# Kernel tuning notes

Measured on AMD Instinct MI355X. Metric: run time of the kernel, lower is better.

Reference implementation:

```python
import jax, jax.numpy as jnp
import numpy as np

B, T, H, L, V = 256, 20, 512, 2, 8964
LQ, LH, LI = 40, 80, 49
BETA = 3.0


def setup_inputs() -> dict:
    key = jax.random.key(0)
    ks = iter(jax.random.split(key, 40))
    s = 1.0 / np.sqrt(H)
    n = lambda shape, sc=s: jax.random.normal(next(ks), shape, jnp.float32) * sc
    inp = {
        'emb': n((B, T, H), 1.0),
        'question': n((B, LQ, 2 * H), 1.0),
        'history': n((B, LH, 2 * H), 1.0),
        'image': n((B, LI, 2 * H), 1.0),
        'h0': jnp.zeros((L, B, H), jnp.float32),
        'c0': jnp.zeros((L, B, H), jnp.float32),
        # LSTM params (both layers have input dim H since ninp == nhid)
        'Wih': n((L, 4 * H, H)), 'Whh': n((L, 4 * H, H)),
        'bih': jnp.zeros((L, 4 * H), jnp.float32), 'bhh': jnp.zeros((L, 4 * H), jnp.float32),
        # question attention: w_q (2H->H), ans_q (H->H), Wa_q (H->1)
        'Wq': n((H, 2 * H)), 'bq': jnp.zeros((H,), jnp.float32),
        'Wansq': n((H, H)), 'bansq': jnp.zeros((H,), jnp.float32),
        'waq': n((1, H)), 'baq': jnp.zeros((1,), jnp.float32),
        # history attention
        'Wh': n((H, 2 * H)), 'bh': jnp.zeros((H,), jnp.float32),
        'Wansh': n((H, H)), 'bansh': jnp.zeros((H,), jnp.float32),
        'wah': n((1, H)), 'bah': jnp.zeros((1,), jnp.float32),
        # image attention
        'Wi': n((H, 2 * H)), 'bi': jnp.zeros((H,), jnp.float32),
        'Wansi': n((H, H)), 'bansi': jnp.zeros((H,), jnp.float32),
        'wai': n((1, H)), 'bai': jnp.zeros((1,), jnp.float32),
        # concat fusion (3H -> H)
        'Wcat': n((H, 3 * H)), 'bcat': jnp.zeros((H,), jnp.float32),
        # decoder SimpleClassifier: 2H -> 4H -> V
        'Wd1': n((4 * H, 2 * H)), 'bd1': jnp.zeros((4 * H,), jnp.float32),
        'Wd2': n((V, 4 * H), 1.0 / np.sqrt(4 * H)), 'bd2': jnp.zeros((V,), jnp.float32),
    }
    return inp


def reference(emb, question, history, image, h0, c0,
              Wih, Whh, bih, bhh,
              Wq, bq, Wansq, bansq, waq, baq,
              Wh, bh, Wansh, bansh, wah, bah,
              Wi, bi, Wansi, bansi, wai, bai,
              Wcat, bcat, Wd1, bd1, Wd2, bd2):
    nlayers = Wih.shape[0]
    # context projections are timestep-invariant: hoist out of the loop
    q_emb = question @ Wq.T + bq   # [B, LQ, H]
    h_emb = history @ Wh.T + bh    # [B, LH, H]
    i_emb = image @ Wi.T + bi      # [B, LI, H]

    def attend(ctx, out, Wans, bans, wa, ba):
        # ctx: [B, Lx, H], out: [B, H]
        a = jnp.tanh(ctx + (out @ Wans.T + bans)[:, None, :])
        logits = jnp.einsum('blh,h->bl', a, wa[0]) + ba[0]
        w = jax.nn.softmax(logits, axis=1)
        return jnp.einsum('bl,blh->bh', w, ctx)

    def step(carry, x_t):
        h, c = carry  # each [L, B, H]
        inp = x_t
        hs, cs = [], []
        for l in range(nlayers):
            gates = inp @ Wih[l].T + h[l] @ Whh[l].T + bih[l] + bhh[l]
            gi, gf, gg, go = jnp.split(gates, 4, axis=-1)  # torch gate order i,f,g,o
            cn = jax.nn.sigmoid(gf) * c[l] + jax.nn.sigmoid(gi) * jnp.tanh(gg)
            hn = jax.nn.sigmoid(go) * jnp.tanh(cn)
            hs.append(hn); cs.append(cn)
            inp = hn
        out = inp  # top-layer output [B, H]
        fq = attend(q_emb, out, Wansq, bansq, waq, baq)
        fh = attend(h_emb, out, Wansh, bansh, wah, bah)
        fi = attend(i_emb, out, Wansi, bansi, wai, bai)
        cat = jnp.tanh(jnp.concatenate([fq, fh, fi], axis=1) @ Wcat.T + bcat)
        fusion = jnp.concatenate([out, cat], axis=1)  # [B, 2H]
        dec = jax.nn.relu(fusion @ Wd1.T + bd1) @ Wd2.T + bd2
        lp = jax.nn.log_softmax(BETA * dec, axis=1)
        return (jnp.stack(hs), jnp.stack(cs)), lp

    (hT, cT), lps = jax.lax.scan(step, (h0, c0), jnp.swapaxes(emb, 0, 1))
    return jnp.swapaxes(lps, 0, 1), hT, cT
```

## Files before the change

kernel.cpp:

```cpp
#include <hip/hip_runtime.h>
#include <cmath>

#define B_ 256
#define T_ 20
#define H_ 512
#define V_ 8964
#define LQ_ 40
#define LH_ 80
#define LI_ 49
#define BT_ (B_ * T_)
#define BH_ (B_ * H_)
#define NPAD_ 9088
#define BETA_ 3.0f

#define MEGA_LSTM_ 128
#define MEGA_CTXQ_ 320
#define MEGA_CTXH_ 640
#define MEGA_CTXI_ 392
#define MEGA_CTX_ (MEGA_CTXQ_ + MEGA_CTXH_ + MEGA_CTXI_)
#define MEGA_GRID_ (MEGA_LSTM_ + MEGA_CTX_)

#define PREP_WCVT_ 2560
#define PREP_WD2_  9088
#define PREP_EMB_  1280
#define PREP_PERM_ 2048
#define PREP_H0_   128
#define PREP_BIAS_ 2
#define PREP_GRID_ (PREP_WCVT_ + PREP_WD2_ + PREP_EMB_ + PREP_PERM_ + PREP_H0_ + PREP_BIAS_)

typedef __attribute__((ext_vector_type(8))) short bf16x8;
typedef __attribute__((ext_vector_type(4))) float f32x4;
typedef __attribute__((ext_vector_type(8))) unsigned short u16x8;

static __device__ __forceinline__ unsigned short f2bf(float f) {
    union { float f; unsigned u; } v; v.f = f;
    unsigned r = v.u + 0x7FFF + ((v.u >> 16) & 1);
    return (unsigned short)(r >> 16);
}
static __device__ __forceinline__ float bf2f(unsigned short u) {
    union { unsigned u; float f; } v; v.u = ((unsigned)u) << 16;
    return v.f;
}
static __device__ __forceinline__ float fast_tanh(float x) {
    const float e = __expf(2.f * x);
    return 1.f - 2.f * __builtin_amdgcn_rcpf(e + 1.f);
}
static __device__ __forceinline__ float fast_sigmoid(float x) {
    return __builtin_amdgcn_rcpf(1.f + __expf(-x));
}
static __device__ __forceinline__ void st16_sc(unsigned short* p, unsigned short v) {
    unsigned int vv = v;
    asm volatile("global_store_short %0, %1, off sc0 sc1" :: "v"(p), "v"(vv) : "memory");
}
static __device__ __forceinline__ int ld32_sc(const int* p) {
    int v;
    asm volatile("global_load_dword %0, %1, off sc0 sc1\n\t"
                 "s_waitcnt vmcnt(0)"
                 : "=v"(v) : "v"(p) : "memory");
    return v;
}
#define GLD16(g, l) __builtin_amdgcn_global_load_lds(                                   \
    (const __attribute__((address_space(1))) unsigned int*)(unsigned long long)(const void*)(g), \
    (__attribute__((address_space(3))) unsigned int*)(unsigned int)(unsigned long long)(void*)(l), \
    16, 0, 0)

static __device__ __forceinline__ u16x8 cvt8(const float* p)
{
    float4 a = *reinterpret_cast<const float4*>(p);
    float4 b = *reinterpret_cast<const float4*>(p + 4);
    u16x8 v;
    v[0] = f2bf(a.x); v[1] = f2bf(a.y); v[2] = f2bf(a.z); v[3] = f2bf(a.w);
    v[4] = f2bf(b.x); v[5] = f2bf(b.y); v[6] = f2bf(b.z); v[7] = f2bf(b.w);
    return v;
}

struct PrepArgs {
    const float* wsrc[8]; unsigned short* wdst[8];
    const float* Wd2; unsigned short* Wd2p;
    const float* emb; unsigned short* emb_bf;
    const float* psrc[4]; unsigned short* pdst[4];
    const float* h0; unsigned short* hbuf;
    const float* bih; const float* bhh; float* bp0; float* bp1;
};

__global__ __launch_bounds__(256) void prep_kernel(PrepArgs a)
{
    static constexpr long long WSZ[8] = {524288, 524288, 524288, 262144,
                                         262144, 262144, 786432, 2097152};
    int g = blockIdx.x;
    const int tid = threadIdx.x;

    if (g < PREP_WCVT_) {
        long long off = (long long)g * 2048;
        int seg = 0;
#pragma unroll
        for (int i = 0; i < 8; ++i)
            if (seg == i && off >= WSZ[i]) { off -= WSZ[i]; ++seg; }
        const long long e = off + (long long)tid * 8;
        *reinterpret_cast<u16x8*>(a.wdst[seg] + e) = cvt8(a.wsrc[seg] + e);
        return;
    }
    g -= PREP_WCVT_;
    if (g < PREP_WD2_) {
        const long long e = (long long)g * 2048 + tid * 8;
        const long long row = e >> 11;
        u16x8 v;
        if (row < V_) v = cvt8(a.Wd2 + e);
        else v = (u16x8)0;
        *reinterpret_cast<u16x8*>(a.Wd2p + e) = v;
        return;
    }
    g -= PREP_WD2_;
    if (g < PREP_EMB_) {
        const long long e = (long long)g * 2048 + tid * 8;
        *reinterpret_cast<u16x8*>(a.emb_bf + e) = cvt8(a.emb + e);
        return;
    }
    g -= PREP_EMB_;
    if (g < PREP_PERM_) {
        const int which = g >> 9;
        const long long e0 = ((long long)(g & 511) * 256 + tid) * 8;
        const int drow = (int)(e0 >> 9);
        const int col = (int)(e0 & 511);
        const int gg = (drow >> 4) & 3;
        const int hsrc = ((drow >> 6) << 4) | (drow & 15);
        const int srow = (gg << 9) | hsrc;
        *reinterpret_cast<u16x8*>(a.pdst[which] + e0) =
            cvt8(a.psrc[which] + (long long)srow * 512 + col);
        return;
    }
    g -= PREP_PERM_;
    if (g < PREP_H0_) {
        const int half = g >> 6;
        const long long e = (long long)(g & 63) * 2048 + tid * 8;
        unsigned short* dst = a.hbuf + (half ? 4LL * BH_ : 0LL);
        *reinterpret_cast<u16x8*>(dst + e) = cvt8(a.h0 + (long long)half * BH_ + e);
        return;
    }
    g -= PREP_H0_;
    {
        const float* b1 = g ? a.bih + 2048 : a.bih;
        const float* b2 = g ? a.bhh + 2048 : a.bhh;
        float* dst = g ? a.bp1 : a.bp0;
#pragma unroll
        for (int i = 0; i < 8; ++i) {
            const int n = i * 256 + tid;
            const int gg = (n >> 4) & 3;
            const int h = ((n >> 6) << 4) | (n & 15);
            const int orig = (gg << 9) | h;
            dst[n] = b1[orig] + b2[orig];
        }
    }
}

static __device__ __forceinline__ int4 ldA8f(const float* A, long long idx)
{
    union { int4 i4; u16x8 v; } r;
    r.v = cvt8(A + idx);
    return r.i4;
}

template <int ACT, int OUTBF, int AF32>
__global__ __launch_bounds__(256, 2) void mfma_gemm(
    const void* __restrict__ A, const unsigned short* __restrict__ W,
    const float* __restrict__ bias1, const float* __restrict__ bias2,
    void* __restrict__ C, long long ldc, int Nreal, int K)
{
    __shared__ __align__(16) unsigned short As[2][128][32];
    __shared__ __align__(16) unsigned short Bs[2][128][32];
    const int tid = threadIdx.x;
    const int lane = tid & 63;
    const int wave = tid >> 6;
    const int wm = wave >> 1, wn = wave & 1;

    const int nwg = gridDim.x * gridDim.y;
    const int orig = blockIdx.y * gridDim.x + blockIdx.x;
    const int xcd = orig & 7, base = orig >> 3;
    const int q8 = nwg >> 3, r8 = nwg & 7;
    const int wg = (xcd < r8 ? xcd * (q8 + 1) : r8 * (q8 + 1) + (xcd - r8) * q8) + base;

    int MI = 8192 / (K << AF32);
    if (MI < 1) MI = 1;
    if (MI > (int)gridDim.y) MI = gridDim.y;
    const int slabSz = gridDim.x * MI;
    const int fullSlabs = gridDim.y / MI;
    const int fullRegion = fullSlabs * slabSz;
    int m0, n0;
    if (wg < fullRegion) {
        const int mb = wg / slabSz, rem = wg % slabSz;
        m0 = (mb * MI + rem % MI) * 128;
        n0 = (rem / MI) * 128;
    } else {
        const int rem = wg - fullRegion;
        const int TM = gridDim.y - fullSlabs * MI;
        m0 = (fullSlabs * MI + rem % TM) * 128;
        n0 = (rem / TM) * 128;
    }

    const int r = tid >> 2;
    const int ck = (tid & 3) * 8;

    const unsigned short* Wp = W + (long long)n0 * K;

    f32x4 acc[4][4] = {};
    int cur = 0;

    if constexpr (!AF32) {
        const unsigned short* Ab = (const unsigned short*)A;
        auto issue = [&](int k0, int buf) {
            const unsigned short* ga0 = Ab + (long long)(m0 + r) * K + k0 + ck;
            const unsigned short* ga1 = Ab + (long long)(m0 + r + 64) * K + k0 + ck;
            const unsigned short* gb0 = Wp + (long long)r * K + k0 + ck;
            const unsigned short* gb1 = Wp + (long long)(r + 64) * K + k0 + ck;
            char* lA = (char*)&As[buf][0][0] + wave * 1024;
            char* lB = (char*)&Bs[buf][0][0] + wave * 1024;
            GLD16(ga0, lA);
            GLD16(ga1, lA + 4096);
            GLD16(gb0, lB);
            GLD16(gb1, lB + 4096);
        };
        issue(0, 0);
        for (int k0 = 0; k0 < K; k0 += 32, cur ^= 1) {
            __syncthreads();
            if (k0 + 32 < K) issue(k0 + 32, cur ^ 1);
            const int lr = lane & 15, lk = (lane >> 4) * 8;
            bf16x8 af[4], bfr[4];
#pragma unroll
            for (int i = 0; i < 4; ++i) {
                af[i]  = *reinterpret_cast<const bf16x8*>(&As[cur][wm * 64 + i * 16 + lr][lk]);
                bfr[i] = *reinterpret_cast<const bf16x8*>(&Bs[cur][wn * 64 + i * 16 + lr][lk]);
            }
#pragma unroll
            for (int i = 0; i < 4; ++i)
#pragma unroll
                for (int j = 0; j < 4; ++j)
                    acc[i][j] = __builtin_amdgcn_mfma_f32_16x16x32_bf16(
                        af[i], bfr[j], acc[i][j], 0, 0, 0);
        }
    } else {
        const float* Af = (const float*)A;
        int4 ra0, ra1, rb0, rb1;
        ra0 = ldA8f(Af, (long long)(m0 + r) * K + ck);
        ra1 = ldA8f(Af, (long long)(m0 + r + 64) * K + ck);
        rb0 = *reinterpret_cast<const int4*>(Wp + (long long)r * K + ck);
        rb1 = *reinterpret_cast<const int4*>(Wp + (long long)(r + 64) * K + ck);
        for (int k0 = 0; k0 < K; k0 += 32, cur ^= 1) {
            *reinterpret_cast<int4*>(&As[cur][r][ck]) = ra0;
            *reinterpret_cast<int4*>(&As[cur][r + 64][ck]) = ra1;
            *reinterpret_cast<int4*>(&Bs[cur][r][ck]) = rb0;
            *reinterpret_cast<int4*>(&Bs[cur][r + 64][ck]) = rb1;
            __syncthreads();
            if (k0 + 32 < K) {
                const int kn = k0 + 32 + ck;
                ra0 = ldA8f(Af, (long long)(m0 + r) * K + kn);
                ra1 = ldA8f(Af, (long long)(m0 + r + 64) * K + kn);
                rb0 = *reinterpret_cast<const int4*>(Wp + (long long)r * K + kn);
                rb1 = *reinterpret_cast<const int4*>(Wp + (long long)(r + 64) * K + kn);
            }
            const int lr = lane & 15, lk = (lane >> 4) * 8;
            bf16x8 af[4], bfr[4];
#pragma unroll
            for (int i = 0; i < 4; ++i) {
                af[i]  = *reinterpret_cast<const bf16x8*>(&As[cur][wm * 64 + i * 16 + lr][lk]);
                bfr[i] = *reinterpret_cast<const bf16x8*>(&Bs[cur][wn * 64 + i * 16 + lr][lk]);
            }
#pragma unroll
            for (int i = 0; i < 4; ++i)
#pragma unroll
                for (int j = 0; j < 4; ++j)
                    acc[i][j] = __builtin_amdgcn_mfma_f32_16x16x32_bf16(
                        af[i], bfr[j], acc[i][j], 0, 0, 0);
        }
    }

    const int lr = lane & 15, lrow4 = (lane >> 4) * 4;
#pragma unroll
    for (int j = 0; j < 4; ++j) {
        const int col = n0 + wn * 64 + j * 16 + lr;
        if (col >= Nreal) continue;
        float bsum = 0.f;
        if (bias1) bsum += bias1[col];
        if (bias2) bsum += bias2[col];
#pragma unroll
        for (int i = 0; i < 4; ++i) {
#pragma unroll
            for (int rr = 0; rr < 4; ++rr) {
                const int row = m0 + wm * 64 + i * 16 + lrow4 + rr;
                float v = acc[i][j][rr] + bsum;
                if (ACT == 1) v = fast_tanh(v);
                if (ACT == 2) v = fmaxf(v, 0.f);
                if (OUTBF)
                    ((unsigned short*)C)[(long long)row * ldc + col] = f2bf(v);
                else
                    ((float*)C)[(long long)row * ldc + col] = v;
            }
        }
    }
}

static void mgemm(hipStream_t s, int act, int outbf, int af32,
                  const void* A, const unsigned short* W,
                  const float* b1, const float* b2,
                  void* C, long long ldc, int M, int Nreal, int K)
{
    dim3 grid((Nreal + 127) / 128, M / 128), blk(256);
#define MG(a, o, f) mfma_gemm<a, o, f><<<grid, blk, 0, s>>>(A, W, b1, b2, C, ldc, Nreal, K)
    if (af32) {
        if (outbf) { if (act == 1) MG(1,1,1); else if (act == 2) MG(2,1,1); else MG(0,1,1); }
        else       { if (act == 1) MG(1,0,1); else if (act == 2) MG(2,0,1); else MG(0,0,1); }
    } else {
        if (outbf) { if (act == 1) MG(1,1,0); else if (act == 2) MG(2,1,0); else MG(0,1,0); }
        else       { if (act == 1) MG(1,0,0); else if (act == 2) MG(2,0,0); else MG(0,0,0); }
    }
#undef MG
}

#define LSTM_ISSUE(b_, dst_) do {                                              \
    const unsigned short* pa_ = (((b_) >> 2) ? q20 : q10) + ((b_) & 3) * 128;  \
    const unsigned short* pb_ = (((b_) >> 2) ? q21 : q11) + ((b_) & 3) * 128;  \
    asm volatile(                                                              \
        "global_load_dwordx4 %0, %[pa], off sc0 sc1\n\t"                       \
        "global_load_dwordx4 %1, %[pa], off offset:64 sc0 sc1\n\t"             \
        "global_load_dwordx4 %2, %[pa], off offset:128 sc0 sc1\n\t"            \
        "global_load_dwordx4 %3, %[pa], off offset:192 sc0 sc1\n\t"            \
        "global_load_dwordx4 %4, %[pb], off sc0 sc1\n\t"                       \
        "global_load_dwordx4 %5, %[pb], off offset:64 sc0 sc1\n\t"             \
        "global_load_dwordx4 %6, %[pb], off offset:128 sc0 sc1\n\t"            \
        "global_load_dwordx4 %7, %[pb], off offset:192 sc0 sc1"                \
        : "=&v"((dst_)[0]), "=&v"((dst_)[1]), "=&v"((dst_)[2]), "=&v"((dst_)[3]), \
          "=&v"((dst_)[4]), "=&v"((dst_)[5]), "=&v"((dst_)[6]), "=&v"((dst_)[7])  \
        : [pa] "v"(pa_), [pb] "v"(pb_)                                         \
        : "memory");                                                           \
} while (0)

__global__ __launch_bounds__(256, 1) void mega_kernel(
    const unsigned short* __restrict__ emb_bf,
    const unsigned short* __restrict__ Wih0p, const unsigned short* __restrict__ Whh0p,
    const unsigned short* __restrict__ Wih1p, const unsigned short* __restrict__ Whh1p,
    const float* __restrict__ bp0, const float* __restrict__ bp1,
    const float* __restrict__ c0,
    unsigned short* __restrict__ hbuf,
    float* __restrict__ st_h, float* __restrict__ st_c,
    unsigned short* __restrict__ h_top,
    int* flags,
    const float* __restrict__ question, const float* __restrict__ history,
    const float* __restrict__ image,
    const unsigned short* __restrict__ Wq_bf, const unsigned short* __restrict__ Wh_bf,
    const unsigned short* __restrict__ Wi_bf,
    const float* __restrict__ bq, const float* __restrict__ bhb,
    const float* __restrict__ bi,
    unsigned short* __restrict__ q_emb, unsigned short* __restrict__ h_emb,
    unsigned short* __restrict__ i_emb)
{
    __shared__ __align__(16) char smem[131072];
    const int gid = blockIdx.x;
    const int tid = threadIdx.x;

    if (gid >= MEGA_LSTM_) {
        int g = gid - MEGA_LSTM_;
        const float* A; const unsigned short* W; const float* bias;
        unsigned short* Cc;
        if (g < MEGA_CTXQ_)       { A = question; W = Wq_bf; bias = bq;  Cc = q_emb; }
        else if (g < MEGA_CTXQ_ + MEGA_CTXH_) {
            g -= MEGA_CTXQ_;        A = history;  W = Wh_bf; bias = bhb; Cc = h_emb; }
        else { g -= MEGA_CTXQ_ + MEGA_CTXH_; A = image; W = Wi_bf; bias = bi; Cc = i_emb; }
        const int m0 = (g >> 2) * 128, n0 = (g & 3) * 128;
        const int K = 1024;

        unsigned short (*As)[128][32] = (unsigned short (*)[128][32])smem;
        unsigned short (*Bs)[128][32] = (unsigned short (*)[128][32])(smem + 16384);
        const int lane = tid & 63;
        const int wave = tid >> 6;
        const int wm = wave >> 1, wn = wave & 1;
        const int r = tid >> 2;
        const int ck = (tid & 3) * 8;
        const unsigned short* Wp = W + (long long)n0 * K;

        f32x4 acc[4][4] = {};
        int4 ra0, ra1, rb0, rb1;
        ra0 = ldA8f(A, (long long)(m0 + r) * K + ck);
        ra1 = ldA8f(A, (long long)(m0 + r + 64) * K + ck);
        rb0 = *reinterpret_cast<const int4*>(Wp + (long long)r * K + ck);
        rb1 = *reinterpret_cast<const int4*>(Wp + (long long)(r + 64) * K + ck);
        int cur = 0;
        for (int k0 = 0; k0 < K; k0 += 32, cur ^= 1) {
            *reinterpret_cast<int4*>(&As[cur][r][ck]) = ra0;
            *reinterpret_cast<int4*>(&As[cur][r + 64][ck]) = ra1;
            *reinterpret_cast<int4*>(&Bs[cur][r][ck]) = rb0;
            *reinterpret_cast<int4*>(&Bs[cur][r + 64][ck]) = rb1;
            __syncthreads();
            if (k0 + 32 < K) {
                const int kn = k0 + 32 + ck;
                ra0 = ldA8f(A, (long long)(m0 + r) * K + kn);
                ra1 = ldA8f(A, (long long)(m0 + r + 64) * K + kn);
                rb0 = *reinterpret_cast<const int4*>(Wp + (long long)r * K + kn);
                rb1 = *reinterpret_cast<const int4*>(Wp + (long long)(r + 64) * K + kn);
            }
            const int lr = lane & 15, lk = (lane >> 4) * 8;
            bf16x8 af[4], bfr[4];
#pragma unroll
            for (int i = 0; i < 4; ++i) {
                af[i]  = *reinterpret_cast<const bf16x8*>(&As[cur][wm * 64 + i * 16 + lr][lk]);
                bfr[i] = *reinterpret_cast<const bf16x8*>(&Bs[cur][wn * 64 + i * 16 + lr][lk]);
            }
#pragma unroll
            for (int i = 0; i < 4; ++i)
#pragma unroll
                for (int j = 0; j < 4; ++j)
                    acc[i][j] = __builtin_amdgcn_mfma_f32_16x16x32_bf16(
                        af[i], bfr[j], acc[i][j], 0, 0, 0);
        }
        const int lr = lane & 15, lrow4 = (lane >> 4) * 4;
#pragma unroll
        for (int j = 0; j < 4; ++j) {
            const int col = n0 + wn * 64 + j * 16 + lr;
            const float bsum = bias[col];
#pragma unroll
            for (int i = 0; i < 4; ++i)
#pragma unroll
                for (int rr = 0; rr < 4; ++rr) {
                    const int row = m0 + wm * 64 + i * 16 + lrow4 + rr;
                    Cc[(long long)row * 512 + col] = f2bf(acc[i][j][rr] + bsum);
                }
        }
        return;
    }

    const int grp = gid >> 6;
    const int id  = gid & 63;
    const int mt = id >> 5, nt = id & 31;
    const int m0 = mt * 128, n0 = nt * 64;
    const int lane = tid & 63;
    const int w = tid >> 6;
    const int lr = lane & 15;
    const int hi = lane >> 4;
    const int hi4 = hi * 4;

    const unsigned short* W1g = (grp ? Wih1p : Wih0p) + (long long)n0 * H_;
    const unsigned short* W2g = (grp ? Whh1p : Whh0p) + (long long)n0 * H_;

#pragma unroll
    for (int it = 0; it < 16; ++it) {
        const int e = (tid + it * 256) * 8;
        const int row = e >> 9, col = e & 511;
        const int bir = (col * 2) ^ ((row & 7) << 4);
        char* dst = smem + row * 1024 + bir;
        *reinterpret_cast<int4*>(dst) =
            *reinterpret_cast<const int4*>(W1g + (long long)row * H_ + col);
        *reinterpret_cast<int4*>(dst + 65536) =
            *reinterpret_cast<const int4*>(W2g + (long long)row * H_ + col);
    }
    __syncthreads();

    const int h = nt * 16 + lr;
    const float* bp = grp ? bp1 : bp0;
    float bg[4];
#pragma unroll
    for (int g = 0; g < 4; ++g) bg[g] = bp[n0 + g * 16 + lr];

    const int ar0 = m0 + w * 32 + lr;
    const int ar1 = ar0 + 16;

    float cregA[4], cregB[4], hn0[4], hn1[4];
#pragma unroll
    for (int rr = 0; rr < 4; ++rr) {
        cregA[rr] = c0[(long long)grp * BH_ + (long long)(m0 + w * 32 + hi4 + rr) * H_ + h];
        cregB[rr] = c0[(long long)grp * BH_ + (long long)(m0 + w * 32 + 16 + hi4 + rr) * H_ + h];
    }

    int bbase[4];
#pragma unroll
    for (int j = 0; j < 4; ++j)
        bbase[j] = (j * 16 + lr) * 1024 + ((hi * 16) ^ ((lr & 3) << 4));
    const int xk6 = ((lr >> 2) & 1) << 6;

    int* myFlag = flags + (mt * 64 + grp * 32 + nt) * 16;
    const long long sEmb = (long long)T_ * H_;

    for (int s = 0; s <= T_; ++s) {
        const bool active = (grp == 0) ? (s < T_) : (s >= 1);
        const int t = grp ? (s - 1) : s;
        if (active) {
            const unsigned short *A1, *A2;
            long long sA1;
            unsigned short* hout;
            if (grp == 0) {
                A1 = emb_bf + (long long)t * H_; sA1 = sEmb;
                A2 = hbuf + (long long)(s % 3) * BH_;
                hout = hbuf + (long long)((s + 1) % 3) * BH_;
            } else {
                A1 = hbuf + (long long)(s % 3) * BH_; sA1 = H_;
                A2 = hbuf + (long long)(3 + (s & 1)) * BH_;
                hout = hbuf + (long long)(3 + ((s + 1) & 1)) * BH_;
            }
            const unsigned short* q10 = A1 + (long long)ar0 * sA1 + hi * 8;
            const unsigned short* q11 = A1 + (long long)ar1 * sA1 + hi * 8;
            const unsigned short* q20 = A2 + (long long)ar0 * H_ + hi * 8;
            const unsigned short* q21 = A2 + (long long)ar1 * H_ + hi * 8;

            int4 buf[3][8];
            LSTM_ISSUE(0, buf[0]);
            LSTM_ISSUE(1, buf[1]);
            LSTM_ISSUE(2, buf[2]);

            f32x4 accA[4] = {}, accB[4] = {};
#pragma unroll
            for (int b = 0; b < 8; ++b) {
                if (b < 6)      asm volatile("s_waitcnt vmcnt(16)" ::: "memory");
                else if (b == 6) asm volatile("s_waitcnt vmcnt(8)" ::: "memory");
                else             asm volatile("s_waitcnt vmcnt(0)" ::: "memory");
                __builtin_amdgcn_sched_barrier(0);
#pragma unroll
                for (int i = 0; i < 4; ++i) {
                    const int it = b * 4 + i;
                    const int kk = it & 15, p = it >> 4;
                    const bf16x8 a0 = *reinterpret_cast<const bf16x8*>(&buf[b % 3][i]);
                    const bf16x8 a1 = *reinterpret_cast<const bf16x8*>(&buf[b % 3][4 + i]);
                    const int kb = ((kk << 6) ^ xk6) + (p << 16);
#pragma unroll
                    for (int j = 0; j < 4; ++j) {
                        const bf16x8 bfv = *reinterpret_cast<const bf16x8*>(
                            smem + bbase[j] + kb);
                        accA[j] = __builtin_amdgcn_mfma_f32_16x16x32_bf16(a0, bfv, accA[j], 0, 0, 0);
                        accB[j] = __builtin_amdgcn_mfma_f32_16x16x32_bf16(a1, bfv, accB[j], 0, 0, 0);
                    }
                }
                if (b + 3 < 8) LSTM_ISSUE(b + 3, buf[b % 3]);
            }

#pragma unroll
            for (int rr = 0; rr < 4; ++rr) {
                {
                    const int b = m0 + w * 32 + hi4 + rr;
                    const float i_ = fast_sigmoid(accA[0][rr] + bg[0]);
                    const float f_ = fast_sigmoid(accA[1][rr] + bg[1]);
                    const float g_ = fast_tanh(accA[2][rr] + bg[2]);
                    const float o_ = fast_sigmoid(accA[3][rr] + bg[3]);
                    const float cn = f_ * cregA[rr] + i_ * g_;
                    const float hn = o_ * fast_tanh(cn);
                    cregA[rr] = cn; hn0[rr] = hn;
                    st16_sc(&hout[(long long)b * H_ + h], f2bf(hn));
                }
                {
                    const int b = m0 + w * 32 + 16 + hi4 + rr;
                    const float i_ = fast_sigmoid(accB[0][rr] + bg[0]);
                    const float f_ = fast_sigmoid(accB[1][rr] + bg[1]);
                    const float g_ = fast_tanh(accB[2][rr] + bg[2]);
                    const float o_ = fast_sigmoid(accB[3][rr] + bg[3]);
                    const float cn = f_ * cregB[rr] + i_ * g_;
                    const float hn = o_ * fast_tanh(cn);
                    cregB[rr] = cn; hn1[rr] = hn;
                    st16_sc(&hout[(long long)b * H_ + h], f2bf(hn));
                }
            }
            if (s == T_) {
#pragma unroll
                for (int rr = 0; rr < 4; ++rr) {
                    const int b0r = m0 + w * 32 + hi4 + rr;
                    const int b1r = b0r + 16;
                    h_top[((long long)b0r * T_ + t) * H_ + h] = f2bf(hn0[rr]);
                    h_top[((long long)b1r * T_ + t) * H_ + h] = f2bf(hn1[rr]);
                    st_h[(long long)grp * BH_ + (long long)b0r * H_ + h] = hn0[rr];
                    st_h[(long long)grp * BH_ + (long long)b1r * H_ + h] = hn1[rr];
                    st_c[(long long)grp * BH_ + (long long)b0r * H_ + h] = cregA[rr];
                    st_c[(long long)grp * BH_ + (long long)b1r * H_ + h] = cregB[rr];
                }
            }
        }
        if (s < T_) {
            __syncthreads();
            if (tid == 0) {
                int v = s + 1;
                asm volatile("global_store_dword %0, %1, off sc0 sc1"
                             :: "v"(myFlag), "v"(v) : "memory");
            }
            if (active) {
#pragma unroll
                for (int rr = 0; rr < 4; ++rr) {
                    const int b0r = m0 + w * 32 + hi4 + rr;
                    const int b1r = b0r + 16;
                    if (grp == 1) {
                        h_top[((long long)b0r * T_ + t) * H_ + h] = f2bf(hn0[rr]);
                        h_top[((long long)b1r * T_ + t) * H_ + h] = f2bf(hn1[rr]);
                    }
                    if (t == T_ - 1) {
                        st_h[(long long)grp * BH_ + (long long)b0r * H_ + h] = hn0[rr];
                        st_h[(long long)grp * BH_ + (long long)b1r * H_ + h] = hn1[rr];
                        st_c[(long long)grp * BH_ + (long long)b0r * H_ + h] = cregA[rr];
                        st_c[(long long)grp * BH_ + (long long)b1r * H_ + h] = cregB[rr];
                    }
                }
            }
            if (tid < 64) {
                const int thr = (grp == 0 && tid >= 32) ? s : s + 1;
                const int* fp = flags + (mt * 64 + tid) * 16;
                while (ld32_sc(fp) < thr) __builtin_amdgcn_s_sleep(2);
            }
            __syncthreads();
        }
    }
}

__global__ __launch_bounds__(256) void attend3_kernel(
    const unsigned short* __restrict__ q_emb, const unsigned short* __restrict__ h_emb,
    const unsigned short* __restrict__ i_emb,
    const float* __restrict__ proj3,
    const float* __restrict__ waq, const float* __restrict__ baq, const float* __restrict__ bansq,
    const float* __restrict__ wah, const float* __restrict__ bah, const float* __restrict__ bansh,
    const float* __restrict__ wai, const float* __restrict__ bai, const float* __restrict__ bansi,
    const unsigned short* __restrict__ h_top,
    unsigned short* __restrict__ fcat, unsigned short* __restrict__ fusion)
{
    __shared__ float p_lds[512];
    __shared__ float wa_lds[512];
    __shared__ float lg[96];
    const int bt0 = blockIdx.x;
    const int bt = (bt0 & 7) * (BT_ / 8) + (bt0 >> 3);
    const int c = blockIdx.y;
    const int b = bt / T_;
    const int tid = threadIdx.x;
    const int wid = tid >> 6, lane = tid & 63;

    if (c == 0 && tid < 64)
        *reinterpret_cast<u16x8*>(&fusion[(long long)bt * 1024 + tid * 8]) =
            *reinterpret_cast<const u16x8*>(&h_top[(long long)bt * 512 + tid * 8]);

    const unsigned short* ctx = c == 0 ? q_emb : c == 1 ? h_emb : i_emb;
    const int Lx = c == 0 ? LQ_ : c == 1 ? LH_ : LI_;
    const float* wa = c == 0 ? waq : c == 1 ? wah : wai;
    const float bav = (c == 0 ? baq : c == 1 ? bah : bai)[0];
    const float* bans = c == 0 ? bansq : c == 1 ? bansh : bansi;

    p_lds[tid]       = proj3[(long long)bt * 1536 + c * 512 + tid] + bans[tid];
    p_lds[tid + 256] = proj3[(long long)bt * 1536 + c * 512 + tid + 256] + bans[tid + 256];
    wa_lds[tid] = wa[tid];
    wa_lds[tid + 256] = wa[tid + 256];
    __syncthreads();

    for (int l = wid; l < Lx; l += 4) {
        const unsigned short* crow = ctx + ((long long)b * Lx + l) * H_;
        float acc = 0.f;
#pragma unroll
        for (int j = 0; j < 8; ++j) {
            const int hp = lane + 64 * j;
            acc += wa_lds[hp] * fast_tanh(bf2f(crow[hp]) + p_lds[hp]);
        }
        for (int o = 32; o > 0; o >>= 1) acc += __shfl_down(acc, o);
        if (lane == 0) lg[l] = acc + bav;
    }
    __syncthreads();
    if (tid == 0) {
        float m = -1e30f;
        for (int l = 0; l < Lx; ++l) m = fmaxf(m, lg[l]);
        float ssum = 0.f;
        for (int l = 0; l < Lx; ++l) { const float e = __expf(lg[l] - m); lg[l] = e; ssum += e; }
        const float inv = __builtin_amdgcn_rcpf(ssum);
        for (int l = 0; l < Lx; ++l) lg[l] *= inv;
    }
    __syncthreads();
    for (int hp = tid; hp < H_; hp += 256) {
        float acc = 0.f;
        for (int l = 0; l < Lx; ++l)
            acc += lg[l] * bf2f(ctx[((long long)b * Lx + l) * H_ + hp]);
        fcat[(long long)bt * 1536 + c * 512 + hp] = f2bf(acc);
    }
}

__global__ __launch_bounds__(256) void log_softmax_kernel(float* __restrict__ out)
{
    __shared__ float red[4];
    __shared__ float bc;
    const long long base = (long long)blockIdx.x * V_;
    const int tid = threadIdx.x, lane = tid & 63, wid = tid >> 6;

    float r[36];
    float m = -1e30f;
#pragma unroll
    for (int i = 0; i < 36; ++i) {
        const int v = tid + i * 256;
        r[i] = (v < V_) ? BETA_ * out[base + v] : -1e30f;
        m = fmaxf(m, r[i]);
    }
    for (int o = 32; o > 0; o >>= 1) m = fmaxf(m, __shfl_down(m, o));
    if (lane == 0) red[wid] = m;
    __syncthreads();
    if (tid == 0)
        bc = fmaxf(fmaxf(red[0], red[1]), fmaxf(red[2], red[3]));
    __syncthreads();
    m = bc;

    float s = 0.f;
#pragma unroll
    for (int i = 0; i < 36; ++i) s += __expf(r[i] - m);
    for (int o = 32; o > 0; o >>= 1) s += __shfl_down(s, o);
    if (lane == 0) red[wid] = s;
    __syncthreads();
    if (tid == 0) bc = m + logf(red[0] + red[1] + red[2] + red[3]);
    __syncthreads();
    const float ls = bc;
#pragma unroll
    for (int i = 0; i < 36; ++i) {
        const int v = tid + i * 256;
        if (v < V_) out[base + v] = r[i] - ls;
    }
}

extern "C" void kernel_launch(void* const* d_in, const int* in_sizes, int n_in,
                              void* d_out_, int out_size, void* d_ws, size_t ws_size,
                              hipStream_t stream)
{
    const float* emb      = (const float*)d_in[0];
    const float* question = (const float*)d_in[1];
    const float* history  = (const float*)d_in[2];
    const float* image    = (const float*)d_in[3];
    const float* h0       = (const float*)d_in[4];
    const float* c0       = (const float*)d_in[5];
    const float* Wih      = (const float*)d_in[6];
    const float* Whh      = (const float*)d_in[7];
    const float* bih      = (const float*)d_in[8];
    const float* bhh      = (const float*)d_in[9];
    const float* Wq    = (const float*)d_in[10]; const float* bq    = (const float*)d_in[11];
    const float* Wansq = (const float*)d_in[12]; const float* bansq = (const float*)d_in[13];
    const float* waq   = (const float*)d_in[14]; const float* baq   = (const float*)d_in[15];
    const float* Wh    = (const float*)d_in[16]; const float* bh    = (const float*)d_in[17];
    const float* Wansh = (const float*)d_in[18]; const float* bansh = (const float*)d_in[19];
    const float* wah   = (const float*)d_in[20]; const float* bah   = (const float*)d_in[21];
    const float* Wi    = (const float*)d_in[22]; const float* bi    = (const float*)d_in[23];
    const float* Wansi = (const float*)d_in[24]; const float* bansi = (const float*)d_in[25];
    const float* wai   = (const float*)d_in[26]; const float* bai   = (const float*)d_in[27];
    const float* Wcat  = (const float*)d_in[28]; const float* bcat  = (const float*)d_in[29];
    const float* Wd1   = (const float*)d_in[30]; const float* bd1   = (const float*)d_in[31];
    const float* Wd2   = (const float*)d_in[32]; const float* bd2   = (const float*)d_in[33];

    float* out = (float*)d_out_;

    int*   flags = (int*)d_ws;
    float* st_h = (float*)((char*)d_ws + 8192);
    float* st_c = st_h + 2LL * BH_;
    float* bp0  = st_c + 2LL * BH_;
    float* bp1  = bp0 + 2048;
    unsigned short* hbuf   = (unsigned short*)(bp1 + 2048);
    unsigned short* Wih0p  = hbuf + 5LL * BH_;
    unsigned short* Whh0p  = Wih0p + 2048LL * H_;
    unsigned short* Wih1p  = Whh0p + 2048LL * H_;
    unsigned short* Whh1p  = Wih1p + 2048LL * H_;
    unsigned short* emb_bf = Whh1p + 2048LL * H_;
    unsigned short* h_top_bf = emb_bf + (long long)BT_ * H_;
    unsigned short* q_emb_bf = h_top_bf + (long long)BT_ * H_;
    unsigned short* h_emb_bf = q_emb_bf + (long long)B_ * LQ_ * H_;
    unsigned short* i_emb_bf = h_emb_bf + (long long)B_ * LH_ * H_;
    unsigned short* dec1_bf  = i_emb_bf + (long long)B_ * LI_ * H_;
    unsigned short* Wd2p_bf  = dec1_bf + (long long)BT_ * 4 * H_;

    unsigned short* Wq_bf    = (unsigned short*)out;
    unsigned short* Wh_bf    = Wq_bf + 524288;
    unsigned short* Wi_bf    = Wh_bf + 524288;
    unsigned short* Wansq_bf = Wi_bf + 524288;
    unsigned short* Wansh_bf = Wansq_bf + 262144;
    unsigned short* Wansi_bf = Wansh_bf + 262144;
    unsigned short* Wcat_bf  = Wansi_bf + 262144;
    unsigned short* Wd1_bf   = Wcat_bf + 786432;
    float* proj3 = (float*)(Wd1_bf + 2097152);
    unsigned short* fcat_bf   = (unsigned short*)(proj3 + (long long)BT_ * 1536);
    unsigned short* fusion_bf = fcat_bf + (long long)BT_ * 1536;

    {
        PrepArgs a;
        a.wsrc[0] = Wq;    a.wdst[0] = Wq_bf;
        a.wsrc[1] = Wh;    a.wdst[1] = Wh_bf;
        a.wsrc[2] = Wi;    a.wdst[2] = Wi_bf;
        a.wsrc[3] = Wansq; a.wdst[3] = Wansq_bf;
        a.wsrc[4] = Wansh; a.wdst[4] = Wansh_bf;
        a.wsrc[5] = Wansi; a.wdst[5] = Wansi_bf;
        a.wsrc[6] = Wcat;  a.wdst[6] = Wcat_bf;
        a.wsrc[7] = Wd1;   a.wdst[7] = Wd1_bf;
        a.Wd2 = Wd2; a.Wd2p = Wd2p_bf;
        a.emb = emb; a.emb_bf = emb_bf;
        a.psrc[0] = Wih;               a.pdst[0] = Wih0p;
        a.psrc[1] = Whh;               a.pdst[1] = Whh0p;
        a.psrc[2] = Wih + 2048LL * H_; a.pdst[2] = Wih1p;
        a.psrc[3] = Whh + 2048LL * H_; a.pdst[3] = Whh1p;
        a.h0 = h0; a.hbuf = hbuf;
        a.bih = bih; a.bhh = bhh; a.bp0 = bp0; a.bp1 = bp1;
        prep_kernel<<<dim3(PREP_GRID_), dim3(256), 0, stream>>>(a);
    }
    hipMemsetAsync(flags, 0, 8192, stream);

    mega_kernel<<<dim3(MEGA_GRID_), dim3(256), 0, stream>>>(
        emb_bf, Wih0p, Whh0p, Wih1p, Whh1p, bp0, bp1, c0,
        hbuf, st_h, st_c, h_top_bf, flags,
        question, history, image, Wq_bf, Wh_bf, Wi_bf, bq, bh, bi,
        q_emb_bf, h_emb_bf, i_emb_bf);

    mgemm(stream, 0, 0, 0, h_top_bf, Wansq_bf, nullptr, nullptr, proj3, 1536, BT_, 1536, H_);
    attend3_kernel<<<dim3(BT_, 3), dim3(256), 0, stream>>>(
        q_emb_bf, h_emb_bf, i_emb_bf, proj3,
        waq, baq, bansq, wah, bah, bansh, wai, bai, bansi,
        h_top_bf, fcat_bf, fusion_bf);

    mgemm(stream, 1, 1, 0, fcat_bf, Wcat_bf, bcat, nullptr, fusion_bf + H_, 2 * H_, BT_, H_, 3 * H_);

    mgemm(stream, 2, 1, 0, fusion_bf, Wd1_bf, bd1, nullptr, dec1_bf, 4 * H_, BT_, 4 * H_, 2 * H_);
    mgemm(stream, 0, 0, 0, dec1_bf, Wd2p_bf, bd2, nullptr, out, V_, BT_, V_, 4 * H_);

    log_softmax_kernel<<<dim3(BT_), dim3(256), 0, stream>>>(out);

    hipMemcpyAsync(out + (long long)BT_ * V_, st_h,
                   4LL * BH_ * sizeof(float), hipMemcpyDeviceToDevice, stream);
}
```

Baseline: 912.9 us.

## Add 256x256-tile double-buffered GEMM with XCD-aware swizzle for vocab projection

```diff
diff --git a/kernel.cpp b/kernel.cpp
--- a/kernel.cpp
+++ b/kernel.cpp
@@ -10,7 +10,7 @@
 #define LI_ 49
 #define BT_ (B_ * T_)
 #define BH_ (B_ * H_)
-#define NPAD_ 9088
+#define NPAD_ 9216
 #define BETA_ 3.0f
 
 #define MEGA_LSTM_ 128
@@ -21,7 +21,7 @@
 #define MEGA_GRID_ (MEGA_LSTM_ + MEGA_CTX_)
 
 #define PREP_WCVT_ 2560
-#define PREP_WD2_  9088
+#define PREP_WD2_  9216
 #define PREP_EMB_  1280
 #define PREP_PERM_ 2048
 #define PREP_H0_   128
@@ -313,6 +313,122 @@
         else       { if (act == 1) MG(1,0,0); else if (act == 2) MG(2,0,0); else MG(0,0,0); }
     }
 #undef MG
+}
+
+__global__ __launch_bounds__(512, 1) void gemm256_kernel(
+    const unsigned short* __restrict__ A, const unsigned short* __restrict__ W,
+    const float* __restrict__ bias, float* __restrict__ C)
+{
+    __shared__ __align__(16) unsigned short As[2][256][64];
+    __shared__ __align__(16) unsigned short Bs[2][256][64];
+    const int tid = threadIdx.x;
+    const int lane = tid & 63;
+    const int wave = tid >> 6;
+    const int wm = wave >> 2, wn = wave & 3;
+    const int lr = lane & 15, hi = lane >> 4;
+    const int K = 2048;
+
+    const int nwg = gridDim.x * gridDim.y;
+    const int orig = blockIdx.y * gridDim.x + blockIdx.x;
+    const int xcd = orig & 7, base = orig >> 3;
+    const int q8 = nwg >> 3, r8 = nwg & 7;
+    const int wg = (xcd < r8 ? xcd * (q8 + 1) : r8 * (q8 + 1) + (xcd - r8) * q8) + base;
+    const int MI = 2;
+    const int slabSz = gridDim.x * MI;
+    int m0, n0;
+    {
+        const int mb = wg / slabSz, rem = wg % slabSz;
+        m0 = (mb * MI + rem % MI) * 256;
+        n0 = (rem / MI) * 256;
+    }
+
+    const int srow = lane >> 3;
+    const int scol = (lane & 7) * 8;
+    auto stage = [&](int kt, int b) {
+#pragma unroll
+        for (int q = 0; q < 4; ++q) {
+            const int c = wave * 4 + q;
+            const unsigned short* ga = A + (long long)(m0 + 8 * c + srow) * K + kt * 64 + scol;
+            GLD16(ga, (char*)&As[b][0][0] + c * 1024);
+        }
+#pragma unroll
+        for (int q = 0; q < 4; ++q) {
+            const int c = wave * 4 + q;
+            const unsigned short* gw = W + (long long)(n0 + 8 * c + srow) * K + kt * 64 + scol;
+            GLD16(gw, (char*)&Bs[b][0][0] + c * 1024);
+        }
+    };
+
+    f32x4 acc[8][4] = {};
+    const int nt = K / 64;
+    stage(0, 0);
+    stage(1, 1);
+
+    for (int t = 0; t < nt; ++t) {
+        const int b = t & 1;
+        if (t + 1 < nt) asm volatile("s_waitcnt vmcnt(8)" ::: "memory");
+        else            asm volatile("s_waitcnt vmcnt(0)" ::: "memory");
+        __builtin_amdgcn_s_barrier();
+
+#pragma unroll
+        for (int p = 0; p < 3; ++p) {
+            const int mh = p & 1, ks = p >> 1;
+            bf16x8 af[4], bfr[4];
+#pragma unroll
+            for (int i = 0; i < 4; ++i) {
+                af[i]  = *reinterpret_cast<const bf16x8*>(
+                    &As[b][wm * 128 + mh * 64 + i * 16 + lr][ks * 32 + hi * 8]);
+                bfr[i] = *reinterpret_cast<const bf16x8*>(
+                    &Bs[b][wn * 64 + i * 16 + lr][ks * 32 + hi * 8]);
+            }
+            __builtin_amdgcn_s_setprio(1);
+#pragma unroll
+            for (int i = 0; i < 4; ++i)
+#pragma unroll
+                for (int j = 0; j < 4; ++j)
+                    acc[mh * 4 + i][j] = __builtin_amdgcn_mfma_f32_16x16x32_bf16(
+                        af[i], bfr[j], acc[mh * 4 + i][j], 0, 0, 0);
+            __builtin_amdgcn_s_setprio(0);
+            __builtin_amdgcn_s_barrier();
+        }
+        {
+            bf16x8 af[4], bfr[4];
+#pragma unroll
+            for (int i = 0; i < 4; ++i) {
+                af[i]  = *reinterpret_cast<const bf16x8*>(
+                    &As[b][wm * 128 + 64 + i * 16 + lr][32 + hi * 8]);
+                bfr[i] = *reinterpret_cast<const bf16x8*>(
+                    &Bs[b][wn * 64 + i * 16 + lr][32 + hi * 8]);
+            }
+            asm volatile("s_waitcnt lgkmcnt(0)" ::: "memory");
+            __builtin_amdgcn_sched_barrier(0);
+            __builtin_amdgcn_s_barrier();
+            if (t + 2 < nt) stage(t + 2, b);
+            __builtin_amdgcn_s_setprio(1);
+#pragma unroll
+            for (int i = 0; i < 4; ++i)
+#pragma unroll
+                for (int j = 0; j < 4; ++j)
+                    acc[4 + i][j] = __builtin_amdgcn_mfma_f32_16x16x32_bf16(
+                        af[i], bfr[j], acc[4 + i][j], 0, 0, 0);
+            __builtin_amdgcn_s_setprio(0);
+        }
+    }
+
+#pragma unroll
+    for (int j = 0; j < 4; ++j) {
+        const int col = n0 + wn * 64 + j * 16 + lr;
+        if (col >= V_) continue;
+        const float bsum = bias[col];
+#pragma unroll
+        for (int i8 = 0; i8 < 8; ++i8) {
+#pragma unroll
+            for (int rr = 0; rr < 4; ++rr) {
+                const int row = m0 + wm * 128 + i8 * 16 + hi * 4 + rr;
+                C[(long long)row * V_ + col] = acc[i8][j][rr] + bsum;
+            }
+        }
+    }
 }
 
 #define LSTM_ISSUE(b_, dst_) do {                                              \
@@ -801,7 +917,8 @@
     mgemm(stream, 1, 1, 0, fcat_bf, Wcat_bf, bcat, nullptr, fusion_bf + H_, 2 * H_, BT_, H_, 3 * H_);
 
     mgemm(stream, 2, 1, 0, fusion_bf, Wd1_bf, bd1, nullptr, dec1_bf, 4 * H_, BT_, 4 * H_, 2 * H_);
-    mgemm(stream, 0, 0, 0, dec1_bf, Wd2p_bf, bd2, nullptr, out, V_, BT_, V_, 4 * H_);
+    gemm256_kernel<<<dim3(NPAD_ / 256, BT_ / 256), dim3(512), 0, stream>>>(
+        dec1_bf, Wd2p_bf, bd2, out);
 
     log_softmax_kernel<<<dim3(BT_), dim3(256), 0, stream>>>(out);
 
```

Measured after the change: 0.9996 ms. 1.09x slower.
